# Kernel optimization log

Measured on AMD Instinct MI355X. Metric: run time of the kernel, lower is better.

Reference implementation:

```python
import jax, jax.numpy as jnp
import numpy as np
from jax.scipy.linalg import solve_triangular

B, T, D = 4, 4096, 1024
H, R, P = 16, 32, 64          # n_heads, rank, d_head
RIDGE = 1e-3
POWER_K = 2
N_PI = 6                       # power-iteration steps


def setup_inputs() -> dict:
    key = jax.random.key(0)
    k0, k1, k2, k3 = jax.random.split(key, 4)
    h = jax.random.normal(k0, (B, T, D), dtype=jnp.float32)
    t_pref = (3 * T) // 4
    prefix_mask = jnp.concatenate(
        [jnp.ones((B, t_pref), jnp.float32), jnp.zeros((B, T - t_pref), jnp.float32)], axis=1)
    s = 1.0 / np.sqrt(D).astype(np.float32)
    Wk = jax.random.normal(k1, (H * R, D), dtype=jnp.float32) * s   # key_proj.weight
    Wq = jax.random.normal(k2, (H * R, D), dtype=jnp.float32) * s   # query_proj.weight
    Wv = jax.random.normal(k3, (H * P, D), dtype=jnp.float32) * s   # value_proj.weight
    eta = jnp.asarray(1.5, jnp.float32)
    ssn_gamma = jnp.asarray(1.0, jnp.float32)
    return {"h": h, "prefix_mask": prefix_mask, "Wk": Wk, "Wq": Wq, "Wv": Wv,
            "eta": eta, "ssn_gamma": ssn_gamma}


def _ska(h, prefix_mask, Wk, Wq, Wv, eta, ssn_gamma):
    b, t, _ = h.shape
    z = (h @ Wk.T).reshape(b, t, H, R)
    zq = (h @ Wq.T).reshape(b, t, H, R)
    v = (h @ Wv.T).reshape(b, t, H, P)

    m = prefix_mask[:, :, None, None]                               # [B,T,1,1]
    z_norms = jnp.linalg.norm(z, axis=-1, keepdims=True)            # [B,T,H,1]
    max_norm = jnp.clip(jnp.max(z_norms, axis=1, keepdims=True), 1e-6)
    z_f = z / max_norm
    zq_f = zq / max_norm

    z_m = z_f * m
    G = jnp.einsum('bthr,bths->bhrs', z_m, z_m)                     # [B,H,R,R]
    m_lag = (prefix_mask[:, :-1] * prefix_mask[:, 1:])[:, :, None, None]
    M_cov = jnp.einsum('bthr,bths->bhrs', z_f[:, 1:] * m_lag, z_f[:, :-1] * m_lag)
    C_v = jnp.einsum('bthp,bthr->bhpr', v * m, z_m)                 # [B,H,P,R]

    G_t = G + RIDGE * jnp.eye(R, dtype=jnp.float32)
    G_sym = 0.5 * (G_t + jnp.swapaxes(G_t, -1, -2))                 # robust-cholesky first attempt
    L = jnp.linalg.cholesky(G_sym)                                  # lower

    Y = solve_triangular(L, M_cov, lower=True)
    Aw_T = solve_triangular(L, jnp.swapaxes(Y, -1, -2), lower=True)
    A_w = jnp.swapaxes(Aw_T, -1, -2)                                # [B,H,R,R]

    # spectral normalization via power iteration (no-grad in original)
    A_sg = jax.lax.stop_gradient(A_w)
    vv = jnp.ones((b, H, R, 1), jnp.float32) / np.sqrt(R)
    for _ in range(N_PI):
        Av = A_sg @ vv
        u = Av / jnp.clip(jnp.linalg.norm(Av, axis=-2, keepdims=True), 1e-8)
        Atu = jnp.swapaxes(A_sg, -1, -2) @ u
        vv = Atu / jnp.clip(jnp.linalg.norm(Atu, axis=-2, keepdims=True), 1e-8)
    sigma_max = jnp.linalg.norm(A_sg @ vv, axis=-2)[..., 0]          # [B,H]
    scale = jnp.clip(sigma_max, 1.0)[..., None, None]
    A_w = A_w / scale
    gamma_safe = jnp.clip(ssn_gamma, 1.0, 1.5)
    A_w = A_w * gamma_safe

    # B_v = cholesky_solve(C_v^T, L)^T
    X = solve_triangular(L, jnp.swapaxes(C_v, -1, -2), lower=True)
    X = solve_triangular(jnp.swapaxes(L, -1, -2), X, lower=False)
    B_v = jnp.swapaxes(X, -1, -2)                                    # [B,H,P,R]

    zq_perm = jnp.transpose(zq_f, (0, 2, 3, 1))                      # [B,H,R,T]
    w_q = solve_triangular(L, zq_perm, lower=True)
    A_filt = A_w
    for _ in range(POWER_K - 1):
        A_filt = A_filt @ A_w
    w_f = A_filt @ w_q
    z_out = L @ w_f                                                   # [B,H,R,T]
    y_hat = jnp.transpose(B_v @ z_out, (0, 3, 1, 2))                  # [B,T,H,P]
    return eta * y_hat


def reference(h, prefix_mask, Wk, Wq, Wv, eta, ssn_gamma):
    return _ska(h, prefix_mask, Wk, Wq, Wv, eta, ssn_gamma)
```

## Files before the change

### kernel.cpp

```cpp
#include <hip/hip_runtime.h>

#define Tq 4096
#define Dq 1024
#define NCOL 2048
#define RIDGEC 1e-3f
#define PSTRIDE 4104

typedef float  f4_t  __attribute__((ext_vector_type(4)));
typedef __bf16 bf8_t __attribute__((ext_vector_type(8)));
typedef unsigned short us4_t __attribute__((ext_vector_type(4)));

typedef __attribute__((address_space(1))) const void* gas_t;
typedef __attribute__((address_space(3))) void* sas_t;

__device__ __forceinline__ unsigned short f2bf(float f){
    unsigned int u = __float_as_uint(f);
    u += 0x7fffu + ((u >> 16) & 1u);
    return (unsigned short)(u >> 16);
}
__device__ __forceinline__ float bf2f(unsigned short u){
    return __uint_as_float(((unsigned int)u) << 16);
}

__global__ __launch_bounds__(256) void k_prep(const float* __restrict__ h,
                                              const float* __restrict__ Wk,
                                              const float* __restrict__ Wq,
                                              const float* __restrict__ Wv,
                                              unsigned short* __restrict__ hbf,
                                              unsigned short* __restrict__ wbf){
    int bx = blockIdx.x;
    if (bx < 16384){
        size_t i = ((size_t)bx*256 + threadIdx.x)*4;
        float4 v = *(const float4*)(h + i);
        us4_t o; o.x=f2bf(v.x); o.y=f2bf(v.y); o.z=f2bf(v.z); o.w=f2bf(v.w);
        *(us4_t*)(hbf + i) = o;
    } else {
        size_t i = ((size_t)(bx - 16384)*256 + threadIdx.x)*4;
        int row = (int)(i >> 10), col = (int)(i & 1023);
        const float* s;
        if (row < 512)       s = Wk + (size_t)row*1024 + col;
        else if (row < 1024) s = Wq + (size_t)(row-512)*1024 + col;
        else                 s = Wv + (size_t)(row-1024)*1024 + col;
        float4 v = *(const float4*)s;
        us4_t o; o.x=f2bf(v.x); o.y=f2bf(v.y); o.z=f2bf(v.z); o.w=f2bf(v.w);
        *(us4_t*)(wbf + i) = o;
    }
}

#define STAGE_A(UI, KC) do { \
    const unsigned short* g_ = Abase + (KC); \
    __builtin_amdgcn_global_load_lds((gas_t)(g_), (sas_t)&Abuf[(UI)*8192 + w*512], 16, 0, 0); \
    __builtin_amdgcn_global_load_lds((gas_t)(g_ + 128*1024), (sas_t)&Abuf[(UI)*8192 + 4096 + w*512], 16, 0, 0); \
} while(0)
#define STAGE_B(UI, KC) do { \
    const unsigned short* g_ = Bbase + (KC); \
    __builtin_amdgcn_global_load_lds((gas_t)(g_), (sas_t)&Bbuf[(UI)*8192 + w*512], 16, 0, 0); \
    __builtin_amdgcn_global_load_lds((gas_t)(g_ + 128*1024), (sas_t)&Bbuf[(UI)*8192 + 4096 + w*512], 16, 0, 0); \
} while(0)
#define FENCE() asm volatile("" ::: "memory")

__global__ __launch_bounds__(512, 2) void k_gemm(const unsigned short* __restrict__ A,
                                                 const unsigned short* __restrict__ Bw,
                                                 unsigned short* __restrict__ zqv){
    __shared__ __align__(16) unsigned short Abuf[4*8192];
    __shared__ __align__(16) unsigned short Bbuf[4*8192];
    const int tid = threadIdx.x, w = tid >> 6, lane = tid & 63;
    const int wr = w >> 2, wc = w & 3;
    const int bid = blockIdx.x;
    const int swz = (bid & 7)*64 + (bid >> 3);
    const int m0 = (swz >> 3)*256, n0 = (swz & 7)*256;

    const int u    = w*64 + (lane ^ ((lane >> 2) & 3));
    const int urow = u >> 2, ucol = (u & 3)*8;
    const unsigned short* Abase = A  + (size_t)(m0 + urow)*Dq + ucol;
    const unsigned short* Bbase = Bw + (size_t)(n0 + urow)*Dq + ucol;

    const int r16 = lane & 15;
    const int kch = ((((lane >> 4)*16) ^ ((lane & 3) << 4)) >> 1);
    const int aRd = (wr*128 + r16)*32 + kch;
    const int bRd = (wc*64  + r16)*32 + kch;

    f4_t acc[8][4];
#pragma unroll
    for (int i=0;i<8;++i)
#pragma unroll
        for (int j=0;j<4;++j) acc[i][j] = (f4_t){0.f,0.f,0.f,0.f};

    STAGE_A(0, 0);  STAGE_B(0, 0);
    STAGE_A(1, 32); STAGE_B(1, 32);
    asm volatile("s_waitcnt vmcnt(4)" ::: "memory");
    __builtin_amdgcn_s_barrier(); FENCE();

    bf8_t aF[4], bF[4];
    for (int t = 0; t < 15; ++t){
        const int p  = t & 1,  np = (t+1) & 1;
        const int a0 = p*2, a1 = p*2 + 1;
        const int kcN = (t+1)*64;

#pragma unroll
        for (int mi=0;mi<4;++mi) aF[mi] = *(const bf8_t*)&Abuf[a0*8192 + aRd + mi*512];
#pragma unroll
        for (int nj=0;nj<4;++nj) bF[nj] = *(const bf8_t*)&Bbuf[a0*8192 + bRd + nj*512];
        STAGE_A(np*2, kcN);
        __builtin_amdgcn_s_barrier(); FENCE();
        __builtin_amdgcn_s_setprio(1);
#pragma unroll
        for (int mi=0;mi<4;++mi)
#pragma unroll
            for (int nj=0;nj<4;++nj)
                acc[mi][nj] = __builtin_amdgcn_mfma_f32_16x16x32_bf16(aF[mi], bF[nj], acc[mi][nj], 0, 0, 0);
        __builtin_amdgcn_s_setprio(0);
        __builtin_amdgcn_s_barrier(); FENCE();

#pragma unroll
        for (int mi=0;mi<4;++mi) aF[mi] = *(const bf8_t*)&Abuf[a0*8192 + aRd + (mi+4)*512];
        STAGE_B(np*2, kcN);
        __builtin_amdgcn_s_barrier(); FENCE();
        __builtin_amdgcn_s_setprio(1);
#pragma unroll
        for (int mi=0;mi<4;++mi)
#pragma unroll
            for (int nj=0;nj<4;++nj)
                acc[mi+4][nj] = __builtin_amdgcn_mfma_f32_16x16x32_bf16(aF[mi], bF[nj], acc[mi+4][nj], 0, 0, 0);
        __builtin_amdgcn_s_setprio(0);
        asm volatile("s_waitcnt vmcnt(4)" ::: "memory");
        __builtin_amdgcn_s_barrier(); FENCE();

#pragma unroll
        for (int mi=0;mi<4;++mi) aF[mi] = *(const bf8_t*)&Abuf[a1*8192 + aRd + mi*512];
#pragma unroll
        for (int nj=0;nj<4;++nj) bF[nj] = *(const bf8_t*)&Bbuf[a1*8192 + bRd + nj*512];
        STAGE_A(np*2+1, kcN+32);
        __builtin_amdgcn_s_barrier(); FENCE();
        __builtin_amdgcn_s_setprio(1);
#pragma unroll
        for (int mi=0;mi<4;++mi)
#pragma unroll
            for (int nj=0;nj<4;++nj)
                acc[mi][nj] = __builtin_amdgcn_mfma_f32_16x16x32_bf16(aF[mi], bF[nj], acc[mi][nj], 0, 0, 0);
        __builtin_amdgcn_s_setprio(0);
        __builtin_amdgcn_s_barrier(); FENCE();

#pragma unroll
        for (int mi=0;mi<4;++mi) aF[mi] = *(const bf8_t*)&Abuf[a1*8192 + aRd + (mi+4)*512];
        STAGE_B(np*2+1, kcN+32);
        __builtin_amdgcn_s_barrier(); FENCE();
        __builtin_amdgcn_s_setprio(1);
#pragma unroll
        for (int mi=0;mi<4;++mi)
#pragma unroll
            for (int nj=0;nj<4;++nj)
                acc[mi+4][nj] = __builtin_amdgcn_mfma_f32_16x16x32_bf16(aF[mi], bF[nj], acc[mi+4][nj], 0, 0, 0);
        __builtin_amdgcn_s_setprio(0);
        asm volatile("s_waitcnt vmcnt(4)" ::: "memory");
        __builtin_amdgcn_s_barrier(); FENCE();
    }

    asm volatile("s_waitcnt vmcnt(0)" ::: "memory");
    __builtin_amdgcn_s_barrier(); FENCE();
#pragma unroll
    for (int kh=0; kh<2; ++kh){
        const int ui = 2 + kh;
#pragma unroll
        for (int nj=0;nj<4;++nj) bF[nj] = *(const bf8_t*)&Bbuf[ui*8192 + bRd + nj*512];
#pragma unroll
        for (int half=0; half<2; ++half){
#pragma unroll
            for (int mi=0;mi<4;++mi) aF[mi] = *(const bf8_t*)&Abuf[ui*8192 + aRd + (half*4+mi)*512];
#pragma unroll
            for (int mi=0;mi<4;++mi)
#pragma unroll
                for (int nj=0;nj<4;++nj)
                    acc[half*4+mi][nj] = __builtin_amdgcn_mfma_f32_16x16x32_bf16(aF[mi], bF[nj], acc[half*4+mi][nj], 0, 0, 0);
        }
    }

#pragma unroll
    for (int mi=0;mi<8;++mi){
#pragma unroll
        for (int nj=0;nj<4;++nj){
            const int col = n0 + wc*64 + nj*16 + r16;
            const int rb  = m0 + wr*128 + mi*16 + (lane >> 4)*4;
#pragma unroll
            for (int q=0;q<4;++q)
                zqv[(size_t)(rb+q)*NCOL + col] = f2bf(acc[mi][nj][q]);
        }
    }
}

__global__ __launch_bounds__(256) void k_cov(const unsigned short* __restrict__ zqv,
                                             const float* __restrict__ mask,
                                             float* __restrict__ part){
    __shared__ float Zs[65*32];
    __shared__ float Vs[64*64];
    __shared__ float Msk[66];
    __shared__ float sMx[64];
    const int tid = threadIdx.x, w = tid >> 6, lane = tid & 63;
    const int c = blockIdx.x, bh = blockIdx.y, b = bh >> 4, h = bh & 15;
    const unsigned short* zb = zqv + (size_t)b*Tq*NCOL + h*32;
    const unsigned short* vb = zqv + (size_t)b*Tq*NCOL + 1024 + h*64;
    const float* mb = mask + (size_t)b*Tq;

    const bool isC = lane >= 32;
    const bool isM = (lane >= 16) && (lane < 32);
    const int li = isC ? (lane - 32) : (lane & 15);
    const int i0 = (li >> 2)*8, j0 = (li & 3)*8;
    const float* Xb = isC ? (Vs + i0) : (Zs + 32 + i0);
    const int xst = isC ? 64 : 32;
    const float* Yb = isM ? (Zs + j0) : (Zs + 32 + j0);
    const int slotbase = isC ? (2048 + i0*32 + j0) : ((isM ? 1024 : 0) + i0*32 + j0);

    float acc[8][8];
#pragma unroll
    for (int i=0;i<8;++i)
#pragma unroll
        for (int j=0;j<8;++j) acc[i][j] = 0.f;
    float mxl = 0.f;

    for (int t0 = c*512; t0 < c*512 + 512; t0 += 64){
        __syncthreads();
        for (int i = tid; i < 520; i += 256){
            int r = i >> 3, cc = (i & 7)*4;
            int t = t0 - 1 + r;
            float4 o;
            if (t >= 0){
                us4_t u = *(const us4_t*)(zb + (size_t)t*NCOL + cc);
                o.x = bf2f(u.x); o.y = bf2f(u.y); o.z = bf2f(u.z); o.w = bf2f(u.w);
            } else { o.x=0.f; o.y=0.f; o.z=0.f; o.w=0.f; }
            *(float4*)&Zs[r*32 + cc] = o;
        }
        for (int i = tid; i < 1024; i += 256){
            int rr = i >> 4, cc = (i & 15)*4;
            us4_t u = *(const us4_t*)(vb + (size_t)(t0 + rr)*NCOL + cc);
            float4 o; o.x=bf2f(u.x); o.y=bf2f(u.y); o.z=bf2f(u.z); o.w=bf2f(u.w);
            *(float4*)&Vs[rr*64 + cc] = o;
        }
        if (tid < 65){ int t = t0 - 1 + tid; Msk[tid] = (t >= 0) ? mb[t] : 0.f; }
        __syncthreads();
        if (tid < 64){
            const float4* pr = (const float4*)&Zs[(tid+1)*32];
            float s = 0.f;
#pragma unroll
            for (int q=0;q<8;++q){ float4 v = pr[q]; s += v.x*v.x + v.y*v.y + v.z*v.z + v.w*v.w; }
            mxl = fmaxf(mxl, s);
        }
#pragma unroll 2
        for (int tt = w; tt < 64; tt += 4){
            const float mt = Msk[tt+1], mp = Msk[tt];
            const float m2 = mt*mt, al = mt*mp;
            const float wgt = isM ? (al*al) : m2;
            const float* xp = Xb + tt*xst;
            const float* yp = Yb + tt*32;
            float4 x0 = *(const float4*)xp, x1 = *(const float4*)(xp + 4);
            float4 y0 = *(const float4*)yp, y1 = *(const float4*)(yp + 4);
            float xs[8] = {x0.x*wgt, x0.y*wgt, x0.z*wgt, x0.w*wgt,
                           x1.x*wgt, x1.y*wgt, x1.z*wgt, x1.w*wgt};
            float ys[8] = {y0.x, y0.y, y0.z, y0.w, y1.x, y1.y, y1.z, y1.w};
#pragma unroll
            for (int i=0;i<8;++i)
#pragma unroll
                for (int j=0;j<8;++j) acc[i][j] += xs[i]*ys[j];
        }
    }
    float* Acc = Vs;
    __syncthreads();
    if (tid < 64) sMx[tid] = mxl;
#pragma unroll
    for (int r = 0; r < 4; ++r){
        if (w == r){
            if (r == 0){
#pragma unroll
                for (int i=0;i<8;++i)
#pragma unroll
                    for (int j=0;j<8;++j) Acc[slotbase + i*32 + j] = acc[i][j];
            } else {
#pragma unroll
                for (int i=0;i<8;++i)
#pragma unroll
                    for (int j=0;j<8;++j) Acc[slotbase + i*32 + j] += acc[i][j];
            }
        }
        __syncthreads();
    }
    float* dst = part + ((size_t)c*64 + bh)*PSTRIDE;
    for (int i = tid; i < 4096; i += 256) dst[i] = Acc[i];
    if (tid == 0){
        float m = 0.f;
#pragma unroll
        for (int q=0;q<64;++q) m = fmaxf(m, sMx[q]);
        dst[4096] = m;
    }
}

__global__ __launch_bounds__(256) void k_solve(const float* __restrict__ part,
                                               const float* __restrict__ eta_p,
                                               const float* __restrict__ gam_p,
                                               unsigned short* __restrict__ Ebf){
    __shared__ float sM[1024], sC[2048], sGi[1024], sP[1024], sQ[1024], sT[1024];
    __shared__ float sAug[32*66];
    __shared__ float sv[32], su[32], sw[32], ssc[4];
    const int tid = threadIdx.x, bh = blockIdx.x;
    const size_t pb = (size_t)bh*PSTRIDE;

    float mxx = 0.f;
#pragma unroll
    for (int c = 0; c < 8; ++c) mxx = fmaxf(mxx, part[((size_t)c*64)*PSTRIDE + pb + 4096]);
    const float mn = fmaxf(sqrtf(mxx), 1e-6f);
    const float i1 = 1.f/mn, i2 = i1*i1;

    for (int i = tid; i < 1024; i += 256){
        float a0 = 0.f, a1 = 0.f;
        for (int c = 0; c < 8; ++c){
            const float* p = part + ((size_t)c*64)*PSTRIDE + pb;
            a0 += p[i]; a1 += p[1024 + i];
        }
        sT[i] = a0; sM[i] = a1*i2;
    }
    for (int i = tid; i < 2048; i += 256){
        float a = 0.f;
        for (int c = 0; c < 8; ++c) a += part[((size_t)c*64)*PSTRIDE + pb + 2048 + i];
        sC[i] = a*i1;
    }
    __syncthreads();
    for (int i = tid; i < 1024; i += 256){
        int r = i >> 5, s = i & 31;
        float g = 0.5f*(sT[i] + sT[s*32 + r])*i2 + (r == s ? RIDGEC : 0.f);
        sAug[r*66 + s] = g;
        sAug[r*66 + 32 + s] = (r == s) ? 1.f : 0.f;
    }
    __syncthreads();
    const int gi = tid >> 3, gj0 = (tid & 7)*8;
    for (int p = 0; p < 32; ++p){
        float pivd = sAug[p*66 + p];
        float f    = sAug[gi*66 + p];
        float rp[8];
#pragma unroll
        for (int jj = 0; jj < 8; ++jj) rp[jj] = sAug[p*66 + gj0 + jj];
        __syncthreads();
        float pinv = 1.f/pivd;
        if (gi == p){
#pragma unroll
            for (int jj = 0; jj < 8; ++jj) sAug[p*66 + gj0 + jj] = rp[jj]*pinv;
        } else {
            float fp = f*pinv;
#pragma unroll
            for (int jj = 0; jj < 8; ++jj) sAug[gi*66 + gj0 + jj] -= fp*rp[jj];
        }
        __syncthreads();
    }
    for (int i = tid; i < 1024; i += 256){
        int r = i >> 5, s = i & 31;
        sGi[i] = sAug[r*66 + 32 + s];
    }
    __syncthreads();
    {
        const int r = tid >> 3, s0 = (tid & 7)*4;
        float lrow[32];
#pragma unroll
        for (int q = 0; q < 8; ++q) *(float4*)&lrow[q*4] = *(const float4*)&sM[r*32 + q*4];
        float4 a = (float4){0.f,0.f,0.f,0.f};
        for (int k = 0; k < 32; ++k){
            float4 bb = *(const float4*)&sGi[k*32 + s0];
            a.x += lrow[k]*bb.x; a.y += lrow[k]*bb.y; a.z += lrow[k]*bb.z; a.w += lrow[k]*bb.w;
        }
        *(float4*)&sP[r*32 + s0] = a;
    }
    __syncthreads();
    {
        const int r = tid >> 3, s0 = (tid & 7)*4;
        float lrow[32];
#pragma unroll
        for (int q = 0; q < 8; ++q) *(float4*)&lrow[q*4] = *(const float4*)&sGi[r*32 + q*4];
        float4 a = (float4){0.f,0.f,0.f,0.f};
        for (int k = 0; k < 32; ++k){
            float4 bb = *(const float4*)&sP[k*32 + s0];
            a.x += lrow[k]*bb.x; a.y += lrow[k]*bb.y; a.z += lrow[k]*bb.z; a.w += lrow[k]*bb.w;
        }
        *(float4*)&sQ[r*32 + s0] = a;
    }
    __syncthreads();
    if (tid < 32) sv[tid] = 0.17677669529663687f;
    __syncthreads();
    for (int it = 0; it < 6; ++it){
        if (tid < 32){ float a = 0.f; for (int k = 0; k < 32; ++k) a += sQ[tid*32+k]*sv[k]; su[tid] = a; }
        __syncthreads();
        if (tid < 32){ float a = 0.f; for (int k = 0; k < 32; ++k) a += sM[k*32+tid]*su[k]; sw[tid] = a; }
        __syncthreads();
        if (tid < 32){
            float n2 = 0.f;
#pragma unroll
            for (int k = 0; k < 32; ++k) n2 += sw[k]*sw[k];
            sv[tid] = sw[tid] * (1.f/fmaxf(sqrtf(n2), 1e-8f));
        }
        __syncthreads();
    }
    if (tid < 32){ float a = 0.f; for (int k = 0; k < 32; ++k) a += sQ[tid*32+k]*sv[k]; su[tid] = a; }
    __syncthreads();
    if (tid < 32){ float a = 0.f; for (int k = 0; k < 32; ++k) a += sM[k*32+tid]*su[k]; sw[tid] = a; }
    __syncthreads();
    if (tid == 0){
        float n2 = 0.f;
        for (int k = 0; k < 32; ++k) n2 += sw[k]*sw[k];
        float sigma = sqrtf(sqrtf(n2));
        float gam = fminf(fmaxf(gam_p[0], 1.f), 1.5f);
        float s = gam/fmaxf(sigma, 1.f);
        ssc[0] = eta_p[0]*i1*s*s;
    }
    __syncthreads();
    {
        const int r = tid >> 3, s0 = (tid & 7)*4;
        float lrow[32];
#pragma unroll
        for (int q = 0; q < 8; ++q) *(float4*)&lrow[q*4] = *(const float4*)&sQ[r*32 + q*4];
        float4 a = (float4){0.f,0.f,0.f,0.f};
        for (int k = 0; k < 32; ++k){
            float4 bb = *(const float4*)&sP[k*32 + s0];
            a.x += lrow[k]*bb.x; a.y += lrow[k]*bb.y; a.z += lrow[k]*bb.z; a.w += lrow[k]*bb.w;
        }
        *(float4*)&sT[r*32 + s0] = a;
    }
    __syncthreads();
    {
        const float esc = ssc[0];
        const int r = tid >> 2, s0 = (tid & 3)*8;
        float lrow[32];
#pragma unroll
        for (int q = 0; q < 8; ++q) *(float4*)&lrow[q*4] = *(const float4*)&sC[r*32 + q*4];
        float4 a0 = (float4){0.f,0.f,0.f,0.f}, a1 = (float4){0.f,0.f,0.f,0.f};
        for (int k = 0; k < 32; ++k){
            float4 b0 = *(const float4*)&sT[k*32 + s0];
            float4 b1 = *(const float4*)&sT[k*32 + s0 + 4];
            a0.x += lrow[k]*b0.x; a0.y += lrow[k]*b0.y; a0.z += lrow[k]*b0.z; a0.w += lrow[k]*b0.w;
            a1.x += lrow[k]*b1.x; a1.y += lrow[k]*b1.y; a1.z += lrow[k]*b1.z; a1.w += lrow[k]*b1.w;
        }
        us4_t o0, o1;
        o0.x=f2bf(a0.x*esc); o0.y=f2bf(a0.y*esc); o0.z=f2bf(a0.z*esc); o0.w=f2bf(a0.w*esc);
        o1.x=f2bf(a1.x*esc); o1.y=f2bf(a1.y*esc); o1.z=f2bf(a1.z*esc); o1.w=f2bf(a1.w*esc);
        *(us4_t*)&Ebf[(size_t)bh*2048 + r*32 + s0]     = o0;
        *(us4_t*)&Ebf[(size_t)bh*2048 + r*32 + s0 + 4] = o1;
    }
}

__global__ __launch_bounds__(256) void k_outm(const unsigned short* __restrict__ zqv,
                                              const unsigned short* __restrict__ Ebf,
                                              float* __restrict__ out){
    __shared__ __align__(16) unsigned short Es[2048];
    const int tid = threadIdx.x, w = tid >> 6, lane = tid & 63;
    const int bh = blockIdx.y, b = bh >> 4, h = bh & 15;
    ((float4*)Es)[tid & 255] = ((const float4*)(Ebf + (size_t)bh*2048))[tid & 255];
    __syncthreads();

    const int row16 = lane & 15, klo = (lane >> 4)*8;
    const int t0 = blockIdx.x*128 + w*32;
    const unsigned short* zq = zqv + ((size_t)b*Tq + t0 + row16)*NCOL + 512 + h*32 + klo;
    bf8_t aF0 = *(const bf8_t*)zq;
    bf8_t aF1 = *(const bf8_t*)(zq + (size_t)16*NCOL);

    bf8_t bF[4];
#pragma unroll
    for (int j=0;j<4;++j) bF[j] = *(const bf8_t*)&Es[(j*16 + row16)*32 + klo];

    f4_t acc[2][4];
#pragma unroll
    for (int i=0;i<2;++i)
#pragma unroll
        for (int j=0;j<4;++j) acc[i][j] = (f4_t){0.f,0.f,0.f,0.f};
#pragma unroll
    for (int j=0;j<4;++j){
        acc[0][j] = __builtin_amdgcn_mfma_f32_16x16x32_bf16(aF0, bF[j], acc[0][j], 0, 0, 0);
        acc[1][j] = __builtin_amdgcn_mfma_f32_16x16x32_bf16(aF1, bF[j], acc[1][j], 0, 0, 0);
    }
    const int rbase = (lane >> 4)*4;
#pragma unroll
    for (int half=0; half<2; ++half){
#pragma unroll
        for (int j=0;j<4;++j){
            int col = h*64 + j*16 + row16;
#pragma unroll
            for (int q=0;q<4;++q){
                int t = t0 + half*16 + rbase + q;
                out[((size_t)b*Tq + t)*1024 + col] = acc[half][j][q];
            }
        }
    }
}

extern "C" void kernel_launch(void* const* d_in, const int* in_sizes, int n_in,
                              void* d_out, int out_size, void* d_ws, size_t ws_size,
                              hipStream_t stream) {
    const float* h    = (const float*)d_in[0];
    const float* mask = (const float*)d_in[1];
    const float* Wk   = (const float*)d_in[2];
    const float* Wq   = (const float*)d_in[3];
    const float* Wv   = (const float*)d_in[4];
    const float* eta  = (const float*)d_in[5];
    const float* gam  = (const float*)d_in[6];
    float* out = (float*)d_out;

    char* ws = (char*)d_ws;
    unsigned short* hbf = (unsigned short*)(ws);
    unsigned short* wbf = (unsigned short*)(ws + 33554432);
    unsigned short* zqv = (unsigned short*)(ws + 37748736);
    float*          part= (float*)         (ws + 104857600);
    unsigned short* Ebf = (unsigned short*)(ws + 113262592);

    k_prep <<<18432, 256, 0, stream>>>(h, Wk, Wq, Wv, hbf, wbf);
    k_gemm <<<dim3(512), 512, 0, stream>>>(hbf, wbf, zqv);
    k_cov  <<<dim3(8, 64), 256, 0, stream>>>(zqv, mask, part);
    k_solve<<<64, 256, 0, stream>>>(part, eta, gam, Ebf);
    k_outm <<<dim3(32, 64), 256, 0, stream>>>(zqv, Ebf, out);
}
```

Measured before the change: 304.7 us.

## Restructure projection GEMM LDS staging to 64-wide K tiles with XOR swizzle

```diff
diff --git a/kernel.cpp b/kernel.cpp
--- a/kernel.cpp
+++ b/kernel.cpp
@@ -47,38 +47,52 @@
     }
 }
 
-#define STAGE_A(UI, KC) do { \
-    const unsigned short* g_ = Abase + (KC); \
-    __builtin_amdgcn_global_load_lds((gas_t)(g_), (sas_t)&Abuf[(UI)*8192 + w*512], 16, 0, 0); \
-    __builtin_amdgcn_global_load_lds((gas_t)(g_ + 128*1024), (sas_t)&Abuf[(UI)*8192 + 4096 + w*512], 16, 0, 0); \
-} while(0)
-#define STAGE_B(UI, KC) do { \
-    const unsigned short* g_ = Bbase + (KC); \
-    __builtin_amdgcn_global_load_lds((gas_t)(g_), (sas_t)&Bbuf[(UI)*8192 + w*512], 16, 0, 0); \
-    __builtin_amdgcn_global_load_lds((gas_t)(g_ + 128*1024), (sas_t)&Bbuf[(UI)*8192 + 4096 + w*512], 16, 0, 0); \
-} while(0)
-#define FENCE() asm volatile("" ::: "memory")
+
+#define STG(BUF, SRC, PAR, HF, KC) do{ \
+    const unsigned short* g_ = (SRC) + (HF)*131072 + (KC); \
+    unsigned short* l_ = &BUF[(PAR)*16384 + (HF)*8192 + w*1024]; \
+    __builtin_amdgcn_global_load_lds((gas_t)(g_), (sas_t)l_, 16, 0, 0); \
+    __builtin_amdgcn_global_load_lds((gas_t)(g_ + 8192), (sas_t)(l_ + 512), 16, 0, 0); \
+  }while(0)
+
+#define RDA(MI, CS, PAR)  (*(const bf8_t*)&Abuf[(PAR)*16384 + aBase + (MI)*1024 + (CS)])
+#define RDB(NJ, CS, PAR)  (*(const bf8_t*)&Bbuf[(PAR)*16384 + bBase + (NJ)*1024 + (CS)])
+
+#define BARIN() do{ __builtin_amdgcn_s_barrier(); __builtin_amdgcn_sched_barrier(0); }while(0)
+
+#define MM16(AB) do{ \
+    __builtin_amdgcn_s_setprio(1); \
+    _Pragma("unroll") \
+    for (int mi_=0; mi_<4; ++mi_){ \
+      _Pragma("unroll") \
+      for (int nj_=0; nj_<4; ++nj_) \
+        acc[(AB)+mi_][nj_] = __builtin_amdgcn_mfma_f32_16x16x32_bf16(aF[mi_], bF[nj_], acc[(AB)+mi_][nj_], 0, 0, 0); \
+    } \
+    __builtin_amdgcn_s_setprio(0); \
+  }while(0)
 
 __global__ __launch_bounds__(512, 2) void k_gemm(const unsigned short* __restrict__ A,
                                                  const unsigned short* __restrict__ Bw,
                                                  unsigned short* __restrict__ zqv){
-    __shared__ __align__(16) unsigned short Abuf[4*8192];
-    __shared__ __align__(16) unsigned short Bbuf[4*8192];
+    __shared__ __align__(16) unsigned short Abuf[2*2*128*64];
+    __shared__ __align__(16) unsigned short Bbuf[2*2*128*64];
     const int tid = threadIdx.x, w = tid >> 6, lane = tid & 63;
     const int wr = w >> 2, wc = w & 3;
     const int bid = blockIdx.x;
     const int swz = (bid & 7)*64 + (bid >> 3);
     const int m0 = (swz >> 3)*256, n0 = (swz & 7)*256;
 
-    const int u    = w*64 + (lane ^ ((lane >> 2) & 3));
-    const int urow = u >> 2, ucol = (u & 3)*8;
-    const unsigned short* Abase = A  + (size_t)(m0 + urow)*Dq + ucol;
-    const unsigned short* Bbase = Bw + (size_t)(n0 + urow)*Dq + ucol;
-
-    const int r16 = lane & 15;
-    const int kch = ((((lane >> 4)*16) ^ ((lane & 3) << 4)) >> 1);
-    const int aRd = (wr*128 + r16)*32 + kch;
-    const int bRd = (wc*64  + r16)*32 + kch;
+    const int c0   = w*128 + lane;
+    const int row0 = c0 >> 3;
+    const int swz8 = ((lane & 7) ^ (lane >> 3))*8;
+    const unsigned short* Asrc = A  + (size_t)(m0 + row0)*Dq + swz8;
+    const unsigned short* Bsrc = Bw + (size_t)(n0 + row0)*Dq + swz8;
+
+    const int r16 = lane & 15, kg = lane >> 4;
+    const int cswz0 = ((kg    ) ^ (r16 & 7))*8;
+    const int cswz1 = ((kg + 4) ^ (r16 & 7))*8;
+    const int aBase = wr*8192 + r16*64;
+    const int bBase = (wc >> 1)*8192 + (wc & 1)*4096 + r16*64;
 
     f4_t acc[8][4];
 #pragma unroll
@@ -86,93 +100,116 @@
 #pragma unroll
         for (int j=0;j<4;++j) acc[i][j] = (f4_t){0.f,0.f,0.f,0.f};
 
-    STAGE_A(0, 0);  STAGE_B(0, 0);
-    STAGE_A(1, 32); STAGE_B(1, 32);
-    asm volatile("s_waitcnt vmcnt(4)" ::: "memory");
-    __builtin_amdgcn_s_barrier(); FENCE();
-
     bf8_t aF[4], bF[4];
-    for (int t = 0; t < 15; ++t){
-        const int p  = t & 1,  np = (t+1) & 1;
-        const int a0 = p*2, a1 = p*2 + 1;
-        const int kcN = (t+1)*64;
-
-#pragma unroll
-        for (int mi=0;mi<4;++mi) aF[mi] = *(const bf8_t*)&Abuf[a0*8192 + aRd + mi*512];
-#pragma unroll
-        for (int nj=0;nj<4;++nj) bF[nj] = *(const bf8_t*)&Bbuf[a0*8192 + bRd + nj*512];
-        STAGE_A(np*2, kcN);
-        __builtin_amdgcn_s_barrier(); FENCE();
-        __builtin_amdgcn_s_setprio(1);
+
+    STG(Bbuf, Bsrc, 0, 0, 0);
+    STG(Abuf, Asrc, 0, 0, 0);
+    STG(Abuf, Asrc, 0, 1, 0);
+    STG(Bbuf, Bsrc, 0, 1, 0);
+    STG(Bbuf, Bsrc, 1, 0, 64);
+    asm volatile("s_waitcnt vmcnt(2)" ::: "memory");
+    __builtin_amdgcn_s_barrier();
+    __builtin_amdgcn_sched_barrier(0);
+
+    for (int t = 0; t < 14; ++t){
+        const int par = t & 1, npar = par ^ 1;
+        const int kc1 = (t+1)*64, kc2 = kc1 + 64;
+
+#pragma unroll
+        for (int mi=0;mi<4;++mi) aF[mi] = RDA(mi, cswz0, par);
+#pragma unroll
+        for (int nj=0;nj<4;++nj) bF[nj] = RDB(nj, cswz0, par);
+        STG(Abuf, Asrc, npar, 0, kc1);
+        BARIN(); MM16(0);
+        __builtin_amdgcn_s_barrier();
+
+#pragma unroll
+        for (int mi=0;mi<4;++mi) aF[mi] = RDA(mi+4, cswz0, par);
+        STG(Abuf, Asrc, npar, 1, kc1);
+        BARIN(); MM16(4);
+        __builtin_amdgcn_s_barrier();
+
+#pragma unroll
+        for (int mi=0;mi<4;++mi) aF[mi] = RDA(mi, cswz1, par);
+#pragma unroll
+        for (int nj=0;nj<4;++nj) bF[nj] = RDB(nj, cswz1, par);
+        STG(Bbuf, Bsrc, npar, 1, kc1);
+        BARIN(); MM16(0);
+        __builtin_amdgcn_s_barrier();
+
+#pragma unroll
+        for (int mi=0;mi<4;++mi) aF[mi] = RDA(mi+4, cswz1, par);
+        STG(Bbuf, Bsrc, par, 0, kc2);
+        BARIN(); MM16(4);
+        asm volatile("s_waitcnt vmcnt(2)" ::: "memory");
+        __builtin_amdgcn_s_barrier();
+    }
+
+    {
+        const int par = 0, npar = 1, kc1 = 960;
+#pragma unroll
+        for (int mi=0;mi<4;++mi) aF[mi] = RDA(mi, cswz0, par);
+#pragma unroll
+        for (int nj=0;nj<4;++nj) bF[nj] = RDB(nj, cswz0, par);
+        STG(Abuf, Asrc, npar, 0, kc1);
+        BARIN(); MM16(0);
+        __builtin_amdgcn_s_barrier();
+
+#pragma unroll
+        for (int mi=0;mi<4;++mi) aF[mi] = RDA(mi+4, cswz0, par);
+        STG(Abuf, Asrc, npar, 1, kc1);
+        BARIN(); MM16(4);
+        __builtin_amdgcn_s_barrier();
+
+#pragma unroll
+        for (int mi=0;mi<4;++mi) aF[mi] = RDA(mi, cswz1, par);
+#pragma unroll
+        for (int nj=0;nj<4;++nj) bF[nj] = RDB(nj, cswz1, par);
+        STG(Bbuf, Bsrc, npar, 1, kc1);
+        BARIN(); MM16(0);
+        __builtin_amdgcn_s_barrier();
+
+#pragma unroll
+        for (int mi=0;mi<4;++mi) aF[mi] = RDA(mi+4, cswz1, par);
+        BARIN(); MM16(4);
+        asm volatile("s_waitcnt vmcnt(0)" ::: "memory");
+        __builtin_amdgcn_s_barrier();
+    }
+
+    {
+        const int par = 1;
+#pragma unroll
+        for (int mi=0;mi<4;++mi) aF[mi] = RDA(mi, cswz0, par);
+#pragma unroll
+        for (int nj=0;nj<4;++nj) bF[nj] = RDB(nj, cswz0, par);
 #pragma unroll
         for (int mi=0;mi<4;++mi)
 #pragma unroll
             for (int nj=0;nj<4;++nj)
                 acc[mi][nj] = __builtin_amdgcn_mfma_f32_16x16x32_bf16(aF[mi], bF[nj], acc[mi][nj], 0, 0, 0);
-        __builtin_amdgcn_s_setprio(0);
-        __builtin_amdgcn_s_barrier(); FENCE();
-
-#pragma unroll
-        for (int mi=0;mi<4;++mi) aF[mi] = *(const bf8_t*)&Abuf[a0*8192 + aRd + (mi+4)*512];
-        STAGE_B(np*2, kcN);
-        __builtin_amdgcn_s_barrier(); FENCE();
-        __builtin_amdgcn_s_setprio(1);
+#pragma unroll
+        for (int mi=0;mi<4;++mi) aF[mi] = RDA(mi+4, cswz0, par);
 #pragma unroll
         for (int mi=0;mi<4;++mi)
 #pragma unroll
             for (int nj=0;nj<4;++nj)
                 acc[mi+4][nj] = __builtin_amdgcn_mfma_f32_16x16x32_bf16(aF[mi], bF[nj], acc[mi+4][nj], 0, 0, 0);
-        __builtin_amdgcn_s_setprio(0);
-        asm volatile("s_waitcnt vmcnt(4)" ::: "memory");
-        __builtin_amdgcn_s_barrier(); FENCE();
-
-#pragma unroll
-        for (int mi=0;mi<4;++mi) aF[mi] = *(const bf8_t*)&Abuf[a1*8192 + aRd + mi*512];
-#pragma unroll
-        for (int nj=0;nj<4;++nj) bF[nj] = *(const bf8_t*)&Bbuf[a1*8192 + bRd + nj*512];
-        STAGE_A(np*2+1, kcN+32);
-        __builtin_amdgcn_s_barrier(); FENCE();
-        __builtin_amdgcn_s_setprio(1);
+#pragma unroll
+        for (int mi=0;mi<4;++mi) aF[mi] = RDA(mi, cswz1, par);
+#pragma unroll
+        for (int nj=0;nj<4;++nj) bF[nj] = RDB(nj, cswz1, par);
 #pragma unroll
         for (int mi=0;mi<4;++mi)
 #pragma unroll
             for (int nj=0;nj<4;++nj)
                 acc[mi][nj] = __builtin_amdgcn_mfma_f32_16x16x32_bf16(aF[mi], bF[nj], acc[mi][nj], 0, 0, 0);
-        __builtin_amdgcn_s_setprio(0);
-        __builtin_amdgcn_s_barrier(); FENCE();
-
-#pragma unroll
-        for (int mi=0;mi<4;++mi) aF[mi] = *(const bf8_t*)&Abuf[a1*8192 + aRd + (mi+4)*512];
-        STAGE_B(np*2+1, kcN+32);
-        __builtin_amdgcn_s_barrier(); FENCE();
-        __builtin_amdgcn_s_setprio(1);
+#pragma unroll
+        for (int mi=0;mi<4;++mi) aF[mi] = RDA(mi+4, cswz1, par);
 #pragma unroll
         for (int mi=0;mi<4;++mi)
 #pragma unroll
             for (int nj=0;nj<4;++nj)
                 acc[mi+4][nj] = __builtin_amdgcn_mfma_f32_16x16x32_bf16(aF[mi], bF[nj], acc[mi+4][nj], 0, 0, 0);
-        __builtin_amdgcn_s_setprio(0);
-        asm volatile("s_waitcnt vmcnt(4)" ::: "memory");
-        __builtin_amdgcn_s_barrier(); FENCE();
-    }
-
-    asm volatile("s_waitcnt vmcnt(0)" ::: "memory");
-    __builtin_amdgcn_s_barrier(); FENCE();
-#pragma unroll
-    for (int kh=0; kh<2; ++kh){
-        const int ui = 2 + kh;
-#pragma unroll
-        for (int nj=0;nj<4;++nj) bF[nj] = *(const bf8_t*)&Bbuf[ui*8192 + bRd + nj*512];
-#pragma unroll
-        for (int half=0; half<2; ++half){
-#pragma unroll
-            for (int mi=0;mi<4;++mi) aF[mi] = *(const bf8_t*)&Abuf[ui*8192 + aRd + (half*4+mi)*512];
-#pragma unroll
-            for (int mi=0;mi<4;++mi)
-#pragma unroll
-                for (int nj=0;nj<4;++nj)
-                    acc[half*4+mi][nj] = __builtin_amdgcn_mfma_f32_16x16x32_bf16(aF[mi], bF[nj], acc[half*4+mi][nj], 0, 0, 0);
-        }
     }
 
 #pragma unroll
@@ -187,6 +224,12 @@
         }
     }
 }
+
+#undef STG
+#undef RDA
+#undef RDB
+#undef BARIN
+#undef MM16
 
 __global__ __launch_bounds__(256) void k_cov(const unsigned short* __restrict__ zqv,
                                              const float* __restrict__ mask,
```

Measured after the change: 297.1 us. -2.5%, faster.
